# Optimization experiments

Hardware: AMD Instinct MI355X
Metric: run time of the kernel (lower is better)

The kernel has to match this reference:

```python
import jax, jax.numpy as jnp
import numpy as np

H = 1024   # hidden_size
A = 512    # attention_dim
C = 1000   # num_classes
NB = 5     # branches: l, r, f2l, f2r, h2h
IN = 42    # 21 landmarks * 2 coords per branch


def setup_inputs() -> dict:
    key = jax.random.key(0)
    ks = jax.random.split(key, 17)
    s = 0.02
    def n(k, shape):
        return jax.random.normal(k, shape, dtype=jnp.float32) * s
    return {
        "x": jax.random.normal(ks[0], (1, 133, 2), dtype=jnp.float32),
        # layer-0 LSTM params, stacked over the 5 branches (PyTorch gate order i,f,g,o)
        "W_ih0": n(ks[1], (NB, 4 * H, IN)),
        "W_hh0": n(ks[2], (NB, 4 * H, H)),
        "b_ih0": n(ks[3], (NB, 4 * H)),
        "b_hh0": n(ks[4], (NB, 4 * H)),
        # layer-1 LSTM params
        "W_ih1": n(ks[5], (NB, 4 * H, H)),
        "W_hh1": n(ks[6], (NB, 4 * H, H)),
        "b_ih1": n(ks[7], (NB, 4 * H)),
        "b_hh1": n(ks[8], (NB, 4 * H)),
        # per-branch additive attention
        "Wa": n(ks[9], (NB, A, H)),
        "ba": n(ks[10], (NB, A)),
        "Ws": n(ks[11], (NB, A)),
        "bs": n(ks[12], (NB,)),
        # fusion + classifier
        "fuse_w": n(ks[13], (H, NB * H)),
        "fuse_b": n(ks[14], (H,)),
        "fc_w": n(ks[15], (C, H)),
        "fc_b": n(ks[16], (C,)),
    }


def _prepare_input(x):
    # x: (1, 133, 2) -> (5, 42) branch features. Mirrors prepare_input exactly.
    x0 = x[0]
    body = x0[:17]
    left = x0[91:112]
    right = x0[112:133]
    src_body = x0[0]
    src_left = x0[100]
    src_right = x0[121]
    w_l = left[:, 0].max() - left[:, 0].min()
    h_l = left[:, 1].max() - left[:, 1].min()
    w_r = right[:, 0].max() - right[:, 0].min()
    h_r = right[:, 1].max() - right[:, 1].min()
    w_b = body[5, 0] - body[6, 0]
    h_b = 4.0 * w_b
    f2l = left - src_body
    f2r = right - src_body
    h2h = left - right
    left = left - src_left
    right = right - src_right
    one = jnp.ones((), x.dtype)
    cond_l = (w_l != 0) & (h_l != 0)
    cond_r = (w_r != 0) & (h_r != 0)
    cond_b = (w_b != 0) & (h_b != 0)
    left = left / jnp.stack([jnp.where(cond_l, w_l, one), jnp.where(cond_l, h_l, one)])
    right = right / jnp.stack([jnp.where(cond_r, w_r, one), jnp.where(cond_r, h_r, one)])
    wb = jnp.where(cond_b, w_b, one)
    hb = jnp.where(cond_b, h_b, one)
    f2l = f2l / jnp.stack([wb, one])   # only x-column divided by w_body
    f2r = f2r / jnp.stack([one, hb])   # only y-column divided by h_body
    h2h = h2h / jnp.stack([wb, hb])
    feat = jnp.concatenate([left, right, f2l, f2r, h2h], axis=0)  # (105, 2)
    return feat.reshape(NB, IN)  # split the 210-vector into the 5 branch slices


def _lstm_cell(xi, h, c, Wih, Whh, bih, bhh):
    g = Wih @ xi + bih + Whh @ h + bhh            # (4H,)
    i, f, gg, o = jnp.split(g, 4)
    c2 = jax.nn.sigmoid(f) * c + jax.nn.sigmoid(i) * jnp.tanh(gg)
    h2 = jax.nn.sigmoid(o) * jnp.tanh(c2)
    return h2


def _branch(xi, Wih0, Whh0, bih0, bhh0, Wih1, Whh1, bih1, bhh1, Wa_, ba_, Ws_, bs_):
    z = jnp.zeros((H,), xi.dtype)  # initialize_cell_and_hidden_state -> zeros
    h0 = _lstm_cell(xi, z, z, Wih0, Whh0, bih0, bhh0)
    h1 = _lstm_cell(h0, z, z, Wih1, Whh1, bih1, bhh1)
    # additive attention over the length-1 sequence (softmax over 1 elem == 1)
    aw = jnp.tanh(Wa_ @ h1 + ba_)                 # (A,)
    s = Ws_ @ aw + bs_                            # scalar score
    w = jax.nn.softmax(s.reshape(1))[0]
    return w * h1                                 # context vector (H,)


def _forward(x, W_ih0, W_hh0, b_ih0, b_hh0, W_ih1, W_hh1, b_ih1, b_hh1,
             Wa, ba, Ws, bs, fuse_w, fuse_b, fc_w, fc_b):
    xb = _prepare_input(x)                        # (5, 42)
    ctx = jax.vmap(_branch)(xb, W_ih0, W_hh0, b_ih0, b_hh0,
                            W_ih1, W_hh1, b_ih1, b_hh1, Wa, ba, Ws, bs)  # (5, H)
    fused = fuse_w @ ctx.reshape(NB * H) + fuse_b # (H,)
    logits = fc_w @ fused + fc_b                  # (C,)
    return logits[None, :]                        # (1, C)


def reference(x, W_ih0, W_hh0, b_ih0, b_hh0, W_ih1, W_hh1, b_ih1, b_hh1,
              Wa, ba, Ws, bs, fuse_w, fuse_b, fc_w, fc_b):
    return _forward(x, W_ih0, W_hh0, b_ih0, b_hh0, W_ih1, W_hh1, b_ih1, b_hh1,
                    Wa, ba, Ws, bs, fuse_w, fuse_b, fc_w, fc_b)
```

## Files before the change

kernel.cpp:

```cpp
#include <hip/hip_runtime.h>
#include <math.h>

#define H 1024
#define NB 5
#define IN 42
#define C_OUT 1000

__device__ __forceinline__ float sigmoidf_(float x) {
    return 1.0f / (1.0f + expf(-x));
}

__device__ __forceinline__ float wave_reduce_sum(float v) {
    #pragma unroll
    for (int off = 32; off > 0; off >>= 1) v += __shfl_xor(v, off);
    return v;
}

__global__ void layer0_kernel(const float* __restrict__ x,
                              const float* __restrict__ wih0,
                              const float* __restrict__ bih0,
                              const float* __restrict__ bhh0,
                              float* __restrict__ h0out) {
    __shared__ float slx[21], sly[21], srx[21], sry[21];
    __shared__ float sxb[IN];

    int out0 = blockIdx.x * 4;
    int b = out0 >> 10;

    int t = threadIdx.x;
    if (t < 21) {
        slx[t] = x[(91 + t) * 2 + 0];
        sly[t] = x[(91 + t) * 2 + 1];
        srx[t] = x[(112 + t) * 2 + 0];
        sry[t] = x[(112 + t) * 2 + 1];
    }
    __syncthreads();

    if (t < 21) {
        float lx_min = slx[0], lx_max = slx[0], ly_min = sly[0], ly_max = sly[0];
        float rx_min = srx[0], rx_max = srx[0], ry_min = sry[0], ry_max = sry[0];
        #pragma unroll
        for (int i = 1; i < 21; ++i) {
            lx_min = fminf(lx_min, slx[i]); lx_max = fmaxf(lx_max, slx[i]);
            ly_min = fminf(ly_min, sly[i]); ly_max = fmaxf(ly_max, sly[i]);
            rx_min = fminf(rx_min, srx[i]); rx_max = fmaxf(rx_max, srx[i]);
            ry_min = fminf(ry_min, sry[i]); ry_max = fmaxf(ry_max, sry[i]);
        }
        float w_l = lx_max - lx_min, h_l = ly_max - ly_min;
        float w_r = rx_max - rx_min, h_r = ry_max - ry_min;
        float w_b = x[5 * 2 + 0] - x[6 * 2 + 0];
        float h_b = 4.0f * w_b;
        float sbx = x[0], sby = x[1];
        float slx0 = slx[9], sly0 = sly[9];
        float srx0 = srx[9], sry0 = sry[9];
        bool cond_l = (w_l != 0.0f) && (h_l != 0.0f);
        bool cond_r = (w_r != 0.0f) && (h_r != 0.0f);
        bool cond_b = (w_b != 0.0f) && (h_b != 0.0f);
        float dlx = cond_l ? w_l : 1.0f, dly = cond_l ? h_l : 1.0f;
        float drx = cond_r ? w_r : 1.0f, dry = cond_r ? h_r : 1.0f;
        float wb  = cond_b ? w_b : 1.0f, hb  = cond_b ? h_b : 1.0f;

        float lx = slx[t], ly = sly[t], rx = srx[t], ry = sry[t];
        float vx, vy;
        switch (b) {
            case 0: vx = (lx - slx0) / dlx; vy = (ly - sly0) / dly; break;
            case 1: vx = (rx - srx0) / drx; vy = (ry - sry0) / dry; break;
            case 2: vx = (lx - sbx) / wb;   vy = (ly - sby);        break;
            case 3: vx = (rx - sbx);        vy = (ry - sby) / hb;   break;
            default:vx = (lx - rx) / wb;    vy = (ly - ry) / hb;    break;
        }
        sxb[2 * t + 0] = vx;
        sxb[2 * t + 1] = vy;
    }
    __syncthreads();

    int wave = t >> 6;
    int lane = t & 63;
    int j = (out0 + wave) & (H - 1);

    float xv = (lane < IN) ? sxb[lane] : 0.0f;
    const float* Wb = wih0 + (size_t)b * 4 * H * IN;
    float gi = 0.0f, gg = 0.0f, go = 0.0f;
    if (lane < IN) {
        gi = Wb[(size_t)(j)         * IN + lane] * xv;
        gg = Wb[(size_t)(j + 2 * H) * IN + lane] * xv;
        go = Wb[(size_t)(j + 3 * H) * IN + lane] * xv;
    }
    gi = wave_reduce_sum(gi);
    gg = wave_reduce_sum(gg);
    go = wave_reduce_sum(go);
    if (lane == 0) {
        size_t base = (size_t)b * 4 * H;
        gi += bih0[base + j]         + bhh0[base + j];
        gg += bih0[base + j + 2 * H] + bhh0[base + j + 2 * H];
        go += bih0[base + j + 3 * H] + bhh0[base + j + 3 * H];
        float c2 = sigmoidf_(gi) * tanhf(gg);
        h0out[b * H + j] = sigmoidf_(go) * tanhf(c2);
    }
}

__global__ void layer1_kernel(const float* __restrict__ wih1,
                              const float* __restrict__ bih1,
                              const float* __restrict__ bhh1,
                              const float* __restrict__ h0,
                              float* __restrict__ ctx) {
    __shared__ float4 hs[H / 4];
    int out0 = blockIdx.x * 8;
    int b = out0 >> 10;
    if (threadIdx.x < H / 4)
        hs[threadIdx.x] = ((const float4*)(h0 + b * H))[threadIdx.x];
    __syncthreads();

    int wave = threadIdx.x >> 6;
    int lane = threadIdx.x & 63;
    int j = (out0 + wave) & (H - 1);

    const float* Wb = wih1 + (size_t)b * 4 * H * H;
    const float4* ri = (const float4*)(Wb + (size_t)(j)         * H);
    const float4* rg = (const float4*)(Wb + (size_t)(j + 2 * H) * H);
    const float4* ro = (const float4*)(Wb + (size_t)(j + 3 * H) * H);

    float gi = 0.0f, gg = 0.0f, go = 0.0f;
    #pragma unroll
    for (int k = lane; k < H / 4; k += 64) {
        float4 h = hs[k];
        float4 a = ri[k]; gi += a.x * h.x + a.y * h.y + a.z * h.z + a.w * h.w;
        float4 c = rg[k]; gg += c.x * h.x + c.y * h.y + c.z * h.z + c.w * h.w;
        float4 d = ro[k]; go += d.x * h.x + d.y * h.y + d.z * h.z + d.w * h.w;
    }
    gi = wave_reduce_sum(gi);
    gg = wave_reduce_sum(gg);
    go = wave_reduce_sum(go);
    if (lane == 0) {
        size_t base = (size_t)b * 4 * H;
        gi += bih1[base + j]         + bhh1[base + j];
        gg += bih1[base + j + 2 * H] + bhh1[base + j + 2 * H];
        go += bih1[base + j + 3 * H] + bhh1[base + j + 3 * H];
        float c2 = sigmoidf_(gi) * tanhf(gg);
        ctx[b * H + j] = sigmoidf_(go) * tanhf(c2);
    }
}

__global__ void fuse_kernel(const float* __restrict__ fuse_w,
                            const float* __restrict__ fuse_b,
                            const float* __restrict__ ctx,
                            float* __restrict__ fused) {
    int row = blockIdx.x;
    const float4* r  = (const float4*)(fuse_w + (size_t)row * (NB * H));
    const float4* c4 = (const float4*)ctx;
    float acc = 0.0f;
    #pragma unroll
    for (int k = threadIdx.x; k < (NB * H) / 4; k += 256) {
        float4 a = r[k], c = c4[k];
        acc += a.x * c.x + a.y * c.y + a.z * c.z + a.w * c.w;
    }
    acc = wave_reduce_sum(acc);
    __shared__ float red[4];
    int wave = threadIdx.x >> 6, lane = threadIdx.x & 63;
    if (lane == 0) red[wave] = acc;
    __syncthreads();
    if (threadIdx.x == 0) {
        fused[row] = red[0] + red[1] + red[2] + red[3] + fuse_b[row];
    }
}

__global__ void fc_kernel(const float* __restrict__ fc_w,
                          const float* __restrict__ fc_b,
                          const float* __restrict__ fused,
                          float* __restrict__ out) {
    __shared__ float4 fs[H / 4];
    fs[threadIdx.x] = ((const float4*)fused)[threadIdx.x];
    __syncthreads();
    int wave = threadIdx.x >> 6, lane = threadIdx.x & 63;
    int row = blockIdx.x * 4 + wave;
    const float4* r = (const float4*)(fc_w + (size_t)row * H);
    float acc = 0.0f;
    #pragma unroll
    for (int k = lane; k < H / 4; k += 64) {
        float4 a = r[k], f = fs[k];
        acc += a.x * f.x + a.y * f.y + a.z * f.z + a.w * f.w;
    }
    acc = wave_reduce_sum(acc);
    if (lane == 0) out[row] = acc + fc_b[row];
}

extern "C" void kernel_launch(void* const* d_in, const int* in_sizes, int n_in,
                              void* d_out, int out_size, void* d_ws, size_t ws_size,
                              hipStream_t stream) {
    (void)in_sizes; (void)n_in; (void)out_size; (void)ws_size;
    const float* x      = (const float*)d_in[0];
    const float* W_ih0  = (const float*)d_in[1];
    const float* b_ih0  = (const float*)d_in[3];
    const float* b_hh0  = (const float*)d_in[4];
    const float* W_ih1  = (const float*)d_in[5];
    const float* b_ih1  = (const float*)d_in[7];
    const float* b_hh1  = (const float*)d_in[8];
    const float* fuse_w = (const float*)d_in[13];
    const float* fuse_b = (const float*)d_in[14];
    const float* fc_w   = (const float*)d_in[15];
    const float* fc_b   = (const float*)d_in[16];
    float* out = (float*)d_out;

    float* ws    = (float*)d_ws;
    float* h0    = ws;
    float* ctx   = ws + 5120;
    float* fused = ws + 10240;

    layer0_kernel<<<1280, 256, 0, stream>>>(x, W_ih0, b_ih0, b_hh0, h0);
    layer1_kernel<<<640, 512, 0, stream>>>(W_ih1, b_ih1, b_hh1, h0, ctx);
    fuse_kernel<<<1024, 256, 0, stream>>>(fuse_w, fuse_b, ctx, fused);
    fc_kernel<<<250, 256, 0, stream>>>(fc_w, fc_b, fused, out);
}
```

Baseline: 249.6 us.

## Fuse all stages into one cooperative kernel with weight prefetch before grid syncs

```diff
diff --git a/kernel.cpp b/kernel.cpp
--- a/kernel.cpp
+++ b/kernel.cpp
@@ -1,10 +1,12 @@
 #include <hip/hip_runtime.h>
+#include <hip/hip_cooperative_groups.h>
 #include <math.h>
+
+namespace cg = cooperative_groups;
 
 #define H 1024
 #define NB 5
 #define IN 42
-#define C_OUT 1000
 
 __device__ __forceinline__ float sigmoidf_(float x) {
     return 1.0f / (1.0f + expf(-x));
@@ -16,18 +18,31 @@
     return v;
 }
 
-__global__ void layer0_kernel(const float* __restrict__ x,
-                              const float* __restrict__ wih0,
-                              const float* __restrict__ bih0,
-                              const float* __restrict__ bhh0,
-                              float* __restrict__ h0out) {
+__device__ __forceinline__ float dot4(float4 a, float4 b) {
+    return a.x * b.x + a.y * b.y + a.z * b.z + a.w * b.w;
+}
+
+__global__ void __launch_bounds__(256, 5)
+fused_all(const float* __restrict__ x,
+          const float* __restrict__ wih0, const float* __restrict__ bih0,
+          const float* __restrict__ bhh0,
+          const float* __restrict__ wih1, const float* __restrict__ bih1,
+          const float* __restrict__ bhh1,
+          const float* __restrict__ fuse_w, const float* __restrict__ fuse_b,
+          const float* __restrict__ fc_w, const float* __restrict__ fc_b,
+          float* __restrict__ h0g, float* __restrict__ ctxg,
+          float* __restrict__ fusedg, float* __restrict__ outg)
+{
+    cg::grid_group grid = cg::this_grid();
+    const int q = blockIdx.x;
+    const int t = threadIdx.x;
+    const int wave = t >> 6, lane = t & 63;
+    const int task = q * 4 + wave;
+    const int b = task >> 10;
+    const int j = task & (H - 1);
+
     __shared__ float slx[21], sly[21], srx[21], sry[21];
     __shared__ float sxb[IN];
-
-    int out0 = blockIdx.x * 4;
-    int b = out0 >> 10;
-
-    int t = threadIdx.x;
     if (t < 21) {
         slx[t] = x[(91 + t) * 2 + 0];
         sly[t] = x[(91 + t) * 2 + 1];
@@ -35,7 +50,6 @@
         sry[t] = x[(112 + t) * 2 + 1];
     }
     __syncthreads();
-
     if (t < 21) {
         float lx_min = slx[0], lx_max = slx[0], ly_min = sly[0], ly_max = sly[0];
         float rx_min = srx[0], rx_max = srx[0], ry_min = sry[0], ry_max = sry[0];
@@ -59,7 +73,6 @@
         float dlx = cond_l ? w_l : 1.0f, dly = cond_l ? h_l : 1.0f;
         float drx = cond_r ? w_r : 1.0f, dry = cond_r ? h_r : 1.0f;
         float wb  = cond_b ? w_b : 1.0f, hb  = cond_b ? h_b : 1.0f;
-
         float lx = slx[t], ly = sly[t], rx = srx[t], ry = sry[t];
         float vx, vy;
         switch (b) {
@@ -74,10 +87,161 @@
     }
     __syncthreads();
 
-    int wave = t >> 6;
-    int lane = t & 63;
+    const float* Wb1 = wih1 + (size_t)b * 4 * H * H;
+    const float4* ri1 = (const float4*)(Wb1 + (size_t)(j)         * H);
+    const float4* rg1 = (const float4*)(Wb1 + (size_t)(j + 2 * H) * H);
+    const float4* ro1 = (const float4*)(Wb1 + (size_t)(j + 3 * H) * H);
+    float4 p0 = ri1[lane], p1 = ri1[lane + 64];
+    float4 p2 = rg1[lane], p3 = rg1[lane + 64];
+    float4 p4 = ro1[lane], p5 = ro1[lane + 64];
+
+    {
+        const float* Wb0 = wih0 + (size_t)b * 4 * H * IN;
+        float xv = (lane < IN) ? sxb[lane] : 0.0f;
+        float gi = 0.0f, gg = 0.0f, go = 0.0f;
+        if (lane < IN) {
+            gi = Wb0[(size_t)(j)         * IN + lane] * xv;
+            gg = Wb0[(size_t)(j + 2 * H) * IN + lane] * xv;
+            go = Wb0[(size_t)(j + 3 * H) * IN + lane] * xv;
+        }
+        gi = wave_reduce_sum(gi);
+        gg = wave_reduce_sum(gg);
+        go = wave_reduce_sum(go);
+        if (lane == 0) {
+            size_t base = (size_t)b * 4 * H;
+            gi += bih0[base + j]         + bhh0[base + j];
+            gg += bih0[base + j + 2 * H] + bhh0[base + j + 2 * H];
+            go += bih0[base + j + 3 * H] + bhh0[base + j + 3 * H];
+            float c2 = sigmoidf_(gi) * tanhf(gg);
+            h0g[b * H + j] = sigmoidf_(go) * tanhf(c2);
+        }
+    }
+
+    grid.sync();
+
+    {
+        const float4* h4 = (const float4*)(h0g + b * H);
+        float gi, gg, go;
+        float4 hv = h4[lane];
+        gi = dot4(p0, hv); gg = dot4(p2, hv); go = dot4(p4, hv);
+        hv = h4[lane + 64];
+        gi += dot4(p1, hv); gg += dot4(p3, hv); go += dot4(p5, hv);
+        #pragma unroll
+        for (int k = lane + 128; k < 256; k += 64) {
+            float4 h = h4[k];
+            gi += dot4(ri1[k], h);
+            gg += dot4(rg1[k], h);
+            go += dot4(ro1[k], h);
+        }
+        gi = wave_reduce_sum(gi);
+        gg = wave_reduce_sum(gg);
+        go = wave_reduce_sum(go);
+        if (lane == 0) {
+            size_t base = (size_t)b * 4 * H;
+            gi += bih1[base + j]         + bhh1[base + j];
+            gg += bih1[base + j + 2 * H] + bhh1[base + j + 2 * H];
+            go += bih1[base + j + 3 * H] + bhh1[base + j + 3 * H];
+            float c2 = sigmoidf_(gi) * tanhf(gg);
+            ctxg[b * H + j] = sigmoidf_(go) * tanhf(c2);
+        }
+    }
+
+    float4 cf0, cf1, cf2, cf3, cf4;
+    if (q < 1024) {
+        const float4* fr = (const float4*)(fuse_w + (size_t)q * (NB * H));
+        cf0 = fr[t]; cf1 = fr[t + 256]; cf2 = fr[t + 512];
+        cf3 = fr[t + 768]; cf4 = fr[t + 1024];
+    }
+
+    grid.sync();
+
+    __shared__ float red[4];
+    if (q < 1024) {
+        const float4* c4 = (const float4*)ctxg;
+        float acc = dot4(cf0, c4[t]) + dot4(cf1, c4[t + 256]) +
+                    dot4(cf2, c4[t + 512]) + dot4(cf3, c4[t + 768]) +
+                    dot4(cf4, c4[t + 1024]);
+        acc = wave_reduce_sum(acc);
+        if (lane == 0) red[wave] = acc;
+        __syncthreads();
+        if (t == 0)
+            fusedg[q] = red[0] + red[1] + red[2] + red[3] + fuse_b[q];
+    }
+
+    const int row2 = q * 4 + wave;
+    float4 f0, f1, f2, f3;
+    if (row2 < 1000) {
+        const float4* fr2 = (const float4*)(fc_w + (size_t)row2 * H);
+        f0 = fr2[lane]; f1 = fr2[lane + 64];
+        f2 = fr2[lane + 128]; f3 = fr2[lane + 192];
+    }
+
+    grid.sync();
+
+    if (row2 < 1000) {
+        const float4* f4 = (const float4*)fusedg;
+        float acc = dot4(f0, f4[lane]) + dot4(f1, f4[lane + 64]) +
+                    dot4(f2, f4[lane + 128]) + dot4(f3, f4[lane + 192]);
+        acc = wave_reduce_sum(acc);
+        if (lane == 0) outg[row2] = acc + fc_b[row2];
+    }
+}
+
+__global__ void layer0_kernel(const float* __restrict__ x,
+                              const float* __restrict__ wih0,
+                              const float* __restrict__ bih0,
+                              const float* __restrict__ bhh0,
+                              float* __restrict__ h0out) {
+    __shared__ float slx[21], sly[21], srx[21], sry[21];
+    __shared__ float sxb[IN];
+    int out0 = blockIdx.x * 4;
+    int b = out0 >> 10;
+    int t = threadIdx.x;
+    if (t < 21) {
+        slx[t] = x[(91 + t) * 2 + 0];
+        sly[t] = x[(91 + t) * 2 + 1];
+        srx[t] = x[(112 + t) * 2 + 0];
+        sry[t] = x[(112 + t) * 2 + 1];
+    }
+    __syncthreads();
+    if (t < 21) {
+        float lx_min = slx[0], lx_max = slx[0], ly_min = sly[0], ly_max = sly[0];
+        float rx_min = srx[0], rx_max = srx[0], ry_min = sry[0], ry_max = sry[0];
+        #pragma unroll
+        for (int i = 1; i < 21; ++i) {
+            lx_min = fminf(lx_min, slx[i]); lx_max = fmaxf(lx_max, slx[i]);
+            ly_min = fminf(ly_min, sly[i]); ly_max = fmaxf(ly_max, sly[i]);
+            rx_min = fminf(rx_min, srx[i]); rx_max = fmaxf(rx_max, srx[i]);
+            ry_min = fminf(ry_min, sry[i]); ry_max = fmaxf(ry_max, sry[i]);
+        }
+        float w_l = lx_max - lx_min, h_l = ly_max - ly_min;
+        float w_r = rx_max - rx_min, h_r = ry_max - ry_min;
+        float w_b = x[10] - x[12];
+        float h_b = 4.0f * w_b;
+        float sbx = x[0], sby = x[1];
+        float slx0 = slx[9], sly0 = sly[9];
+        float srx0 = srx[9], sry0 = sry[9];
+        bool cond_l = (w_l != 0.0f) && (h_l != 0.0f);
+        bool cond_r = (w_r != 0.0f) && (h_r != 0.0f);
+        bool cond_b = (w_b != 0.0f) && (h_b != 0.0f);
+        float dlx = cond_l ? w_l : 1.0f, dly = cond_l ? h_l : 1.0f;
+        float drx = cond_r ? w_r : 1.0f, dry = cond_r ? h_r : 1.0f;
+        float wb  = cond_b ? w_b : 1.0f, hb  = cond_b ? h_b : 1.0f;
+        float lx = slx[t], ly = sly[t], rx = srx[t], ry = sry[t];
+        float vx, vy;
+        switch (b) {
+            case 0: vx = (lx - slx0) / dlx; vy = (ly - sly0) / dly; break;
+            case 1: vx = (rx - srx0) / drx; vy = (ry - sry0) / dry; break;
+            case 2: vx = (lx - sbx) / wb;   vy = (ly - sby);        break;
+            case 3: vx = (rx - sbx);        vy = (ry - sby) / hb;   break;
+            default:vx = (lx - rx) / wb;    vy = (ly - ry) / hb;    break;
+        }
+        sxb[2 * t + 0] = vx;
+        sxb[2 * t + 1] = vy;
+    }
+    __syncthreads();
+    int wave = t >> 6, lane = t & 63;
     int j = (out0 + wave) & (H - 1);
-
     float xv = (lane < IN) ? sxb[lane] : 0.0f;
     const float* Wb = wih0 + (size_t)b * 4 * H * IN;
     float gi = 0.0f, gg = 0.0f, go = 0.0f;
@@ -110,23 +274,19 @@
     if (threadIdx.x < H / 4)
         hs[threadIdx.x] = ((const float4*)(h0 + b * H))[threadIdx.x];
     __syncthreads();
-
-    int wave = threadIdx.x >> 6;
-    int lane = threadIdx.x & 63;
+    int wave = threadIdx.x >> 6, lane = threadIdx.x & 63;
     int j = (out0 + wave) & (H - 1);
-
     const float* Wb = wih1 + (size_t)b * 4 * H * H;
     const float4* ri = (const float4*)(Wb + (size_t)(j)         * H);
     const float4* rg = (const float4*)(Wb + (size_t)(j + 2 * H) * H);
     const float4* ro = (const float4*)(Wb + (size_t)(j + 3 * H) * H);
-
     float gi = 0.0f, gg = 0.0f, go = 0.0f;
     #pragma unroll
     for (int k = lane; k < H / 4; k += 64) {
         float4 h = hs[k];
-        float4 a = ri[k]; gi += a.x * h.x + a.y * h.y + a.z * h.z + a.w * h.w;
-        float4 c = rg[k]; gg += c.x * h.x + c.y * h.y + c.z * h.z + c.w * h.w;
-        float4 d = ro[k]; go += d.x * h.x + d.y * h.y + d.z * h.z + d.w * h.w;
+        gi += dot4(ri[k], h);
+        gg += dot4(rg[k], h);
+        go += dot4(ro[k], h);
     }
     gi = wave_reduce_sum(gi);
     gg = wave_reduce_sum(gg);
@@ -151,17 +311,15 @@
     float acc = 0.0f;
     #pragma unroll
     for (int k = threadIdx.x; k < (NB * H) / 4; k += 256) {
-        float4 a = r[k], c = c4[k];
-        acc += a.x * c.x + a.y * c.y + a.z * c.z + a.w * c.w;
+        acc += dot4(r[k], c4[k]);
     }
     acc = wave_reduce_sum(acc);
     __shared__ float red[4];
     int wave = threadIdx.x >> 6, lane = threadIdx.x & 63;
     if (lane == 0) red[wave] = acc;
     __syncthreads();
-    if (threadIdx.x == 0) {
+    if (threadIdx.x == 0)
         fused[row] = red[0] + red[1] + red[2] + red[3] + fuse_b[row];
-    }
 }
 
 __global__ void fc_kernel(const float* __restrict__ fc_w,
@@ -177,8 +335,7 @@
     float acc = 0.0f;
     #pragma unroll
     for (int k = lane; k < H / 4; k += 64) {
-        float4 a = r[k], f = fs[k];
-        acc += a.x * f.x + a.y * f.y + a.z * f.z + a.w * f.w;
+        acc += dot4(r[k], fs[k]);
     }
     acc = wave_reduce_sum(acc);
     if (lane == 0) out[row] = acc + fc_b[row];
@@ -206,8 +363,21 @@
     float* ctx   = ws + 5120;
     float* fused = ws + 10240;
 
-    layer0_kernel<<<1280, 256, 0, stream>>>(x, W_ih0, b_ih0, b_hh0, h0);
-    layer1_kernel<<<640, 512, 0, stream>>>(W_ih1, b_ih1, b_hh1, h0, ctx);
-    fuse_kernel<<<1024, 256, 0, stream>>>(fuse_w, fuse_b, ctx, fused);
-    fc_kernel<<<250, 256, 0, stream>>>(fc_w, fc_b, fused, out);
-}
+    int nb = 0;
+    hipError_t occ_err = hipOccupancyMaxActiveBlocksPerMultiprocessor(
+        &nb, fused_all, 256, 0);
+
+    if (occ_err == hipSuccess && nb >= 5) {
+        void* args[] = { (void*)&x, (void*)&W_ih0, (void*)&b_ih0, (void*)&b_hh0,
+                         (void*)&W_ih1, (void*)&b_ih1, (void*)&b_hh1,
+                         (void*)&fuse_w, (void*)&fuse_b, (void*)&fc_w, (void*)&fc_b,
+                         (void*)&h0, (void*)&ctx, (void*)&fused, (void*)&out };
+        hipLaunchCooperativeKernel((void*)fused_all, dim3(1280), dim3(256),
+                                   args, 0, stream);
+    } else {
+        layer0_kernel<<<1280, 256, 0, stream>>>(x, W_ih0, b_ih0, b_hh0, h0);
+        layer1_kernel<<<640, 512, 0, stream>>>(W_ih1, b_ih1, b_hh1, h0, ctx);
+        fuse_kernel<<<1024, 256, 0, stream>>>(fuse_w, fuse_b, ctx, fused);
+        fc_kernel<<<250, 256, 0, stream>>>(fc_w, fc_b, fused, out);
+    }
+}
```

Result: no change. 250.7 us (+0.4%).
